# Kernel tuning notes

Hardware: AMD Instinct MI355X
Metric: run time of the kernel (lower is better)

The kernel has to match this reference:

```python
import jax, jax.numpy as jnp
import numpy as np

B, NPG, K, HID, MAXZ = 512, 256, 60, 128, 1000
NTOT = B * NPG            # 131072 nodes
DEG = 16
E = NTOT * DEG            # 2097152 edges
TLD = HID * 3 + 1         # 385 = total_latent_dim
DENSE = (K // 2 - 5 + 1) * 32  # 832


def setup_inputs() -> dict:
    key = jax.random.key(0)
    ks = jax.random.split(key, 20)
    # within-graph random edges, offset per graph
    loc = jax.random.randint(ks[0], (2, B, NPG * DEG), 0, NPG)
    offs = (jnp.arange(B) * NPG)[None, :, None]
    edge_index = (loc + offs).reshape(2, E).astype(jnp.int32)
    z = jax.random.randint(ks[1], (NTOT,), 0, MAXZ).astype(jnp.int32)
    edge_weight = jax.random.uniform(ks[2], (E,), dtype=jnp.float32)
    z_table = jax.random.normal(ks[3], (MAXZ, HID), dtype=jnp.float32) * 0.1
    W0 = jax.random.normal(ks[4], (HID, HID)) * 0.05
    W1 = jax.random.normal(ks[5], (HID, HID)) * 0.05
    W2 = jax.random.normal(ks[6], (HID, HID)) * 0.05
    W3 = jax.random.normal(ks[7], (HID, 1)) * 0.05
    b0 = jnp.zeros((HID,)); b1 = jnp.zeros((HID,)); b2 = jnp.zeros((HID,)); b3 = jnp.zeros((1,))
    conv1_w = jax.random.normal(ks[8], (16, 1, TLD)) * 0.05
    conv1_b = jnp.zeros((16,))
    conv2_w = jax.random.normal(ks[9], (32, 16, 5)) * 0.05
    conv2_b = jnp.zeros((32,))
    lin1_w = jax.random.normal(ks[10], (DENSE, 128)) * 0.05
    lin1_b = jnp.zeros((128,))
    lin2_w = jax.random.normal(ks[11], (128, 1)) * 0.05
    lin2_b = jnp.zeros((1,))
    return {"z_table": z_table, "W0": W0, "b0": b0, "W1": W1, "b1": b1,
            "W2": W2, "b2": b2, "W3": W3, "b3": b3,
            "conv1_w": conv1_w, "conv1_b": conv1_b, "conv2_w": conv2_w, "conv2_b": conv2_b,
            "lin1_w": lin1_w, "lin1_b": lin1_b, "lin2_w": lin2_w, "lin2_b": lin2_b,
            "edge_weight": edge_weight, "z": z, "edge_index": edge_index}


def reference(z_table, W0, b0, W1, b1, W2, b2, W3, b3,
              conv1_w, conv1_b, conv2_w, conv2_b,
              lin1_w, lin1_b, lin2_w, lin2_b,
              edge_weight, z, edge_index):
    # --- GCN normalization with self loops (symmetric) ---
    loops = jnp.arange(NTOT, dtype=edge_index.dtype)
    src = jnp.concatenate([edge_index[0], loops])
    dst = jnp.concatenate([edge_index[1], loops])
    ew = jnp.concatenate([edge_weight, jnp.ones((NTOT,), edge_weight.dtype)])
    deg = jax.ops.segment_sum(ew, dst, num_segments=NTOT)
    dinv = jnp.where(deg > 0, jax.lax.rsqrt(jnp.maximum(deg, 1e-12)), 0.0)
    norm = dinv[src] * ew * dinv[dst]

    def gcn(x, W, b):
        h = x @ W
        agg = jax.ops.segment_sum(h[src] * norm[:, None], dst, num_segments=NTOT)
        return agg + b

    x = z_table[z]                              # [NTOT, HID]
    xs = []
    for (W, b) in ((W0, b0), (W1, b1), (W2, b2), (W3, b3)):
        x = jnp.tanh(gcn(x, W, b))
        xs.append(x)
    x = jnp.concatenate(xs, axis=-1)            # [NTOT, 385]

    # --- global sort pool (descending by last channel, top-k per graph) ---
    xg = x.reshape(B, NPG, TLD)
    idx = jnp.argsort(-xg[:, :, -1], axis=1)[:, :K]
    pooled = jnp.take_along_axis(xg, idx[:, :, None], axis=1)   # [B, K, 385]
    y = pooled.reshape(B, 1, K * TLD)

    # --- dense conv1d / MLP head ---
    y = jax.lax.conv_general_dilated(y, conv1_w, (TLD,), 'VALID',
                                     dimension_numbers=('NCH', 'OIH', 'NCH'))
    y = jax.nn.relu(y + conv1_b[None, :, None])                  # [B,16,K]
    y = y.reshape(B, 16, K // 2, 2).max(axis=-1)                 # maxpool(2,2)
    y = jax.lax.conv_general_dilated(y, conv2_w, (1,), 'VALID',
                                     dimension_numbers=('NCH', 'OIH', 'NCH'))
    y = jax.nn.relu(y + conv2_b[None, :, None])                  # [B,32,26]
    y = y.reshape(B, -1)                                         # [B,832]
    y = jax.nn.relu(y @ lin1_w + lin1_b)
    return y @ lin2_w + lin2_b                                   # [B,1]
```

## Files before the change

kernel.cpp:

```cpp
#include <hip/hip_runtime.h>
#include <math.h>

#define NTOT   131072
#define NPG    256
#define BGR    512
#define HID    128
#define EDG    2097152
#define EPG    4096
#define EPGP   4864
#define KTOP   60
#define TLDIM  385

__device__ __forceinline__ int physX(int row, int c4) {
    return (c4 + row + (row >> 3)) & 31;
}
__device__ __forceinline__ int physA(int row, int c4) {
    return (c4 + (row >> 3) + ((row & 1) << 2)) & 31;
}

__global__ __launch_bounds__(1024, 4) void k_gnn(
        const float* __restrict__ zt, const int* __restrict__ z,
        const int* __restrict__ ei, const float* __restrict__ ew,
        const float* __restrict__ W0, const float* __restrict__ b0,
        const float* __restrict__ W1, const float* __restrict__ b1,
        const float* __restrict__ W2, const float* __restrict__ b2,
        const float* __restrict__ W3, const float* __restrict__ b3,
        float* __restrict__ X0, float* __restrict__ X1, float* __restrict__ X2,
        float* __restrict__ keyb, int* __restrict__ sel) {
    __shared__ float4 XS[NPG * 32];
    __shared__ __align__(16) float wnL[EPGP];
    __shared__ __align__(4) unsigned char esrcL[EPGP];
    __shared__ unsigned short offL[NPG + 1];
    __shared__ unsigned short mLn[NPG];
    __shared__ int    cntL[NPG];
    __shared__ float  selfnL[NPG];
    __shared__ float  dinvL[NPG];
    __shared__ float  t3s[NPG];
    __shared__ float  keyL[NPG];

    int t = threadIdx.x;
    int g = blockIdx.x;

    float*          ewL  = (float*)XS;
    unsigned char*  srcB = (unsigned char*)XS + 16384;
    unsigned char*  dstB = (unsigned char*)XS + 20480;
    unsigned short* hh   = (unsigned short*)((char*)XS + 24576);

    for (int j = t; j < EPG; j += 1024) {
        int e = g * EPG + j;
        ewL[j]  = ew[e];
        srcB[j] = (unsigned char)(ei[e] & (NPG - 1));
        dstB[j] = (unsigned char)(ei[EDG + e] & (NPG - 1));
    }
    for (int i = t; i < 64 * 256; i += 1024) hh[i] = 0;
    __syncthreads();
    if (t < 64) {
        int base = t * 64;
        unsigned short* hr = hh + t * 256;
        for (int i = 0; i < 64; i++) hr[dstB[base + i]]++;
    }
    __syncthreads();
    if (t < NPG) {
        int tot = 0;
        for (int c = 0; c < 64; c++) tot += hh[c * 256 + t];
        mLn[t]  = (unsigned short)tot;
        cntL[t] = (tot + 3) & ~3;
    }
    __syncthreads();
    if (t < 64) {
        int carry = 0;
        if (t == 0) offL[0] = 0;
        for (int seg = 0; seg < 4; seg++) {
            int v = cntL[seg * 64 + t];
#pragma unroll
            for (int d = 1; d < 64; d <<= 1) {
                int u = __shfl_up(v, d);
                if (t >= d) v += u;
            }
            offL[seg * 64 + t + 1] = (unsigned short)(v + carry);
            carry += __shfl(v, 63);
        }
    }
    __syncthreads();
    if (t < NPG) {
        int run = offL[t];
        for (int c = 0; c < 64; c++) {
            int tmp = hh[c * 256 + t];
            hh[c * 256 + t] = (unsigned short)run;
            run += tmp;
        }
    }
    __syncthreads();
    if (t < 64) {
        int base = t * 64;
        unsigned short* hr = hh + t * 256;
        for (int i = 0; i < 64; i++) {
            int e = base + i;
            int d = dstB[e];
            int slot = hr[d];
            hr[d] = (unsigned short)(slot + 1);
            esrcL[slot] = srcB[e];
            wnL[slot]   = ewL[e];
        }
    }
    __syncthreads();
    if (t < NPG) {
        int o = offL[t], m = mLn[t];
        float s = 0.f;
        for (int i = 0; i < m; i++) s += wnL[o + i];
        float dv = 1.0f / sqrtf(s + 1.0f);
        dinvL[t]  = dv;
        selfnL[t] = dv * dv;
    }
    __syncthreads();
    if (t < NPG) {
        int o = offL[t], m = mLn[t], pc = cntL[t];
        float dn = dinvL[t];
        for (int i = 0; i < m; i++)
            wnL[o + i] = dinvL[esrcL[o + i]] * wnL[o + i] * dn;
        for (int i = m; i < pc; i++) {
            esrcL[o + i] = (unsigned char)t;
            wnL[o + i]   = 0.f;
        }
    }
    __syncthreads();
    for (int i = t; i < NPG * 32; i += 1024) {
        int row = i >> 5, c4 = i & 31;
        int zi = z[g * NPG + row];
        XS[row * 32 + physX(row, c4)] = ((const float4*)zt)[(size_t)zi * 32 + c4];
    }
    __syncthreads();

    const unsigned int* esrcW = (const unsigned int*)esrcL;
    const float4*       wn4   = (const float4*)wnL;
    int wid  = t >> 6;
    int l    = t & 63;
    int half = l >> 5;
    int c4   = l & 31;
    int rg   = t & 31;
    int cgq  = t >> 5;

#pragma unroll 1
    for (int layer = 0; layer < 3; layer++) {
        const float* W    = (layer == 0) ? W0 : (layer == 1) ? W1 : W2;
        const float* bias = (layer == 0) ? b0 : (layer == 1) ? b1 : b2;
        float* Xout       = (layer == 0) ? X0 : (layer == 1) ? X1 : X2;

        float4 accA[8];
#pragma unroll 1
        for (int it = 0; it < 8; it++) {
            int p    = wid * 8 + it;
            int node = 2 * p + half;
            int oA = offL[2 * p], oM = offL[2 * p + 1], oE = offL[2 * p + 2];
            int m4A = (oM - oA) >> 2, m4B = (oE - oM) >> 2;
            int mmax4 = m4A > m4B ? m4A : m4B;
            int o4 = (half ? oM : oA) >> 2;
            int m4 = half ? m4B : m4A;
            unsigned int selfpack = (unsigned int)node * 0x01010101u;
            float4 acc = make_float4(0.f, 0.f, 0.f, 0.f);

            unsigned int s_cur = selfpack, s_nxt = selfpack;
            float4 w_cur = make_float4(0.f, 0.f, 0.f, 0.f);
            float4 w_nxt = make_float4(0.f, 0.f, 0.f, 0.f);
            float4 v0, v1, v2, v3;
            if (mmax4 > 0) {
                {
                    int jc = (0 < m4) ? 0 : 0;
                    int idx = o4 + jc;
                    unsigned int ss = esrcW[idx]; float4 ww = wn4[idx];
                    if (0 >= m4) { ss = selfpack; ww = make_float4(0.f,0.f,0.f,0.f); }
                    s_cur = ss; w_cur = ww;
                }
                {
                    int jc = (1 < m4) ? 1 : (m4 > 0 ? m4 - 1 : 0);
                    int idx = o4 + jc;
                    unsigned int ss = esrcW[idx]; float4 ww = wn4[idx];
                    if (1 >= m4) { ss = selfpack; ww = make_float4(0.f,0.f,0.f,0.f); }
                    s_nxt = ss; w_nxt = ww;
                }
                int a0 =  s_cur        & 255, a1 = (s_cur >> 8)  & 255;
                int a2i = (s_cur >> 16) & 255, a3 = (s_cur >> 24) & 255;
                v0 = XS[a0 * 32 + physX(a0, c4)];
                v1 = XS[a1 * 32 + physX(a1, c4)];
                v2 = XS[a2i * 32 + physX(a2i, c4)];
                v3 = XS[a3 * 32 + physX(a3, c4)];
            }
            for (int j4 = 0; j4 < mmax4; j4++) {
                int b0i =  s_nxt        & 255, b1i = (s_nxt >> 8)  & 255;
                int b2i = (s_nxt >> 16) & 255, b3i = (s_nxt >> 24) & 255;
                float4 n0 = XS[b0i * 32 + physX(b0i, c4)];
                float4 n1 = XS[b1i * 32 + physX(b1i, c4)];
                float4 n2 = XS[b2i * 32 + physX(b2i, c4)];
                float4 n3 = XS[b3i * 32 + physX(b3i, c4)];
                int jn = j4 + 2;
                int jc = (jn < m4) ? jn : (m4 > 0 ? m4 - 1 : 0);
                int idx = o4 + jc;
                unsigned int s2_ = esrcW[idx];
                float4 w2_ = wn4[idx];
                if (jn >= m4) { s2_ = selfpack; w2_ = make_float4(0.f,0.f,0.f,0.f); }
                acc.x += w_cur.x * v0.x; acc.y += w_cur.x * v0.y;
                acc.z += w_cur.x * v0.z; acc.w += w_cur.x * v0.w;
                acc.x += w_cur.y * v1.x; acc.y += w_cur.y * v1.y;
                acc.z += w_cur.y * v1.z; acc.w += w_cur.y * v1.w;
                acc.x += w_cur.z * v2.x; acc.y += w_cur.z * v2.y;
                acc.z += w_cur.z * v2.z; acc.w += w_cur.z * v2.w;
                acc.x += w_cur.w * v3.x; acc.y += w_cur.w * v3.y;
                acc.z += w_cur.w * v3.z; acc.w += w_cur.w * v3.w;
                v0 = n0; v1 = n1; v2 = n2; v3 = n3;
                w_cur = w_nxt; s_nxt = s2_; w_nxt = w2_;
            }
            float wsf = selfnL[node];
            float4 sv = XS[node * 32 + physX(node, c4)];
            acc.x += wsf * sv.x; acc.y += wsf * sv.y;
            acc.z += wsf * sv.z; acc.w += wsf * sv.w;
            accA[it] = acc;
        }
        __syncthreads();
#pragma unroll
        for (int it = 0; it < 8; it++) {
            int node = 2 * (wid * 8 + it) + half;
            XS[node * 32 + physA(node, c4)] = accA[it];
        }
        __syncthreads();

        float a2[8][4];
#pragma unroll
        for (int i = 0; i < 8; i++)
#pragma unroll
            for (int j = 0; j < 4; j++) a2[i][j] = 0.f;
        for (int k4 = 0; k4 < 32; k4++) {
            float4 a4[8];
#pragma unroll
            for (int i = 0; i < 8; i++) {
                int rl = rg * 8 + i;
                a4[i] = XS[rl * 32 + physA(rl, k4)];
            }
            float4 wv[4];
#pragma unroll
            for (int kw = 0; kw < 4; kw++)
                wv[kw] = *(((const float4*)(W + (size_t)(k4 * 4 + kw) * HID)) + cgq);
#pragma unroll
            for (int kw = 0; kw < 4; kw++) {
#pragma unroll
                for (int i = 0; i < 8; i++) {
                    float a = (kw == 0) ? a4[i].x : (kw == 1) ? a4[i].y
                            : (kw == 2) ? a4[i].z : a4[i].w;
                    a2[i][0] += a * wv[kw].x; a2[i][1] += a * wv[kw].y;
                    a2[i][2] += a * wv[kw].z; a2[i][3] += a * wv[kw].w;
                }
            }
        }
        float4 bv = ((const float4*)bias)[cgq];
        float4 oo[8];
#pragma unroll
        for (int i = 0; i < 8; i++) {
            oo[i].x = tanhf(a2[i][0] + bv.x); oo[i].y = tanhf(a2[i][1] + bv.y);
            oo[i].z = tanhf(a2[i][2] + bv.z); oo[i].w = tanhf(a2[i][3] + bv.w);
        }
        __syncthreads();
#pragma unroll
        for (int i = 0; i < 8; i++) {
            int rl = rg * 8 + i;
            XS[rl * 32 + physX(rl, cgq)] = oo[i];
        }
        __syncthreads();
        for (int i = t; i < NPG * 32; i += 1024) {
            int row = i >> 5, cc = i & 31;
            ((float4*)Xout)[(size_t)g * NPG * 32 + i] = XS[row * 32 + physX(row, cc)];
        }
    }

    {
        int n = t >> 2, part = t & 3;
        const float4* w4 = (const float4*)W3;
        const float4* rb = XS + n * 32;
        float s = 0.f;
#pragma unroll
        for (int q = 0; q < 8; q++) {
            float4 v = rb[physX(n, part * 8 + q)];
            float4 ww = w4[part * 8 + q];
            s += v.x * ww.x + v.y * ww.y + v.z * ww.z + v.w * ww.w;
        }
        s += __shfl_down(s, 2, 4);
        s += __shfl_down(s, 1, 4);
        if (part == 0) t3s[n] = s;
    }
    __syncthreads();

    if (t < NPG) {
        int o = offL[t], m2 = mLn[t];
        float s = 0.f;
        for (int i = 0; i < m2; i++)
            s += wnL[o + i] * t3s[esrcL[o + i]];
        s += selfnL[t] * t3s[t];
        float key = tanhf(s + b3[0]);
        keyL[t] = key;
        keyb[g * NPG + t] = key;
    }
    __syncthreads();
    if (t < NPG) {
        float ki = keyL[t];
        int rank = 0;
        for (int j = 0; j < NPG; j++) {
            float kj = keyL[j];
            rank += (kj > ki) || (kj == ki && j < t);
        }
        if (rank < KTOP) sel[g * KTOP + rank] = g * NPG + t;
    }
}

__global__ __launch_bounds__(256) void k_head(const float* __restrict__ X0,
                                              const float* __restrict__ X1,
                                              const float* __restrict__ X2,
                                              const float* __restrict__ key,
                                              const int* __restrict__ sel,
                                              const float* __restrict__ c1w,
                                              const float* __restrict__ c1b,
                                              const float* __restrict__ c2w,
                                              const float* __restrict__ c2b,
                                              const float* __restrict__ l1w,
                                              const float* __restrict__ l1b,
                                              const float* __restrict__ l2w,
                                              const float* __restrict__ l2b,
                                              float* __restrict__ out) {
    __shared__ __align__(16) float pch[KTOP * 132];
    __shared__ __align__(16) float w1s[16 * 132];
    __shared__ int   seln[KTOP];
    __shared__ float selk[KTOP];
    __shared__ float c1s[16 * KTOP];
    __shared__ float mps[16 * 30];
    __shared__ float w2s[32 * 80];
    __shared__ float yb[832];
    __shared__ float l1p[256];
    __shared__ float l1v[128];

    int g = blockIdx.x, t = threadIdx.x;
    if (t < KTOP) {
        int nd = sel[g * KTOP + t];
        seln[t] = nd;
        selk[t] = key[nd];
    }

    float acc1[4] = {0.f, 0.f, 0.f, 0.f};
    for (int tc = 0; tc < 3; tc++) {
        const float* Xsrc = (tc == 0) ? X0 : ((tc == 1) ? X1 : X2);
        __syncthreads();
        for (int i = t; i < KTOP * 32; i += 256) {
            int k = i >> 5, q = i & 31;
            int nd = seln[k];
            *((float4*)&pch[k * 132 + q * 4]) = ((const float4*)Xsrc)[(size_t)nd * 32 + q];
        }
        for (int i = t; i < 16 * 128; i += 256) {
            int ch = i >> 7, tt = i & 127;
            w1s[ch * 132 + tt] = c1w[ch * TLDIM + tc * 128 + tt];
        }
        __syncthreads();
#pragma unroll
        for (int it = 0; it < 4; it++) {
            int e = it * 256 + t;
            if (e < 960) {
                int k = e >> 4, ch = e & 15;
                const float* pr = &pch[k * 132];
                const float* wr = &w1s[ch * 132];
                float s = 0.f;
#pragma unroll
                for (int q = 0; q < 32; q++) {
                    float4 pv = *((float4*)&pr[q * 4]);
                    float4 wv = *((float4*)&wr[q * 4]);
                    s += pv.x * wv.x + pv.y * wv.y + pv.z * wv.z + pv.w * wv.w;
                }
                acc1[it] += s;
            }
        }
    }
    __syncthreads();
#pragma unroll
    for (int it = 0; it < 4; it++) {
        int e = it * 256 + t;
        if (e < 960) {
            int k = e >> 4, ch = e & 15;
            float v = acc1[it] + selk[k] * c1w[ch * TLDIM + 384] + c1b[ch];
            c1s[ch * KTOP + k] = fmaxf(v, 0.f);
        }
    }
    for (int i = t; i < 2560; i += 256) w2s[i] = c2w[i];
    __syncthreads();
    for (int i = t; i < 480; i += 256) {
        int ch = i / 30, p = i - ch * 30;
        mps[ch * 30 + p] = fmaxf(c1s[ch * KTOP + 2 * p], c1s[ch * KTOP + 2 * p + 1]);
    }
    __syncthreads();
    for (int e = t; e < 832; e += 256) {
        int oc = e / 26, q = e - oc * 26;
        float s = 0.f;
#pragma unroll
        for (int ic = 0; ic < 16; ic++) {
            const float* mr = &mps[ic * 30 + q];
            const float* wr = &w2s[oc * 80 + ic * 5];
#pragma unroll
            for (int j = 0; j < 5; j++) s += mr[j] * wr[j];
        }
        yb[e] = fmaxf(s + c2b[oc], 0.f);
    }
    __syncthreads();
    {
        int u = t & 127, h = t >> 7;
        float s = 0.f;
        for (int d = h * 416; d < h * 416 + 416; d++) s += yb[d] * l1w[d * 128 + u];
        l1p[t] = s;
    }
    __syncthreads();
    if (t < 128) {
        float v = fmaxf(l1p[t] + l1p[t + 128] + l1b[t], 0.f);
        l1v[t] = v * l2w[t];
    }
    __syncthreads();
    if (t < 64) {
        float v = l1v[t] + l1v[t + 64];
        v += __shfl_down(v, 32);
        v += __shfl_down(v, 16);
        v += __shfl_down(v, 8);
        v += __shfl_down(v, 4);
        v += __shfl_down(v, 2);
        v += __shfl_down(v, 1);
        if (t == 0) out[g] = v + l2b[0];
    }
}

extern "C" void kernel_launch(void* const* d_in, const int* in_sizes, int n_in,
                              void* d_out, int out_size, void* d_ws, size_t ws_size,
                              hipStream_t stream) {
    (void)in_sizes; (void)n_in; (void)out_size; (void)ws_size;
    const float* zt  = (const float*)d_in[0];
    const float* W0  = (const float*)d_in[1];
    const float* b0  = (const float*)d_in[2];
    const float* W1  = (const float*)d_in[3];
    const float* b1  = (const float*)d_in[4];
    const float* W2  = (const float*)d_in[5];
    const float* b2  = (const float*)d_in[6];
    const float* W3  = (const float*)d_in[7];
    const float* b3  = (const float*)d_in[8];
    const float* c1w = (const float*)d_in[9];
    const float* c1b = (const float*)d_in[10];
    const float* c2w = (const float*)d_in[11];
    const float* c2b = (const float*)d_in[12];
    const float* l1w = (const float*)d_in[13];
    const float* l1b = (const float*)d_in[14];
    const float* l2w = (const float*)d_in[15];
    const float* l2b = (const float*)d_in[16];
    const float* ew  = (const float*)d_in[17];
    const int*   z   = (const int*)d_in[18];
    const int*   ei  = (const int*)d_in[19];
    float* out = (float*)d_out;

    char* wsp = (char*)d_ws;
    size_t off = 0;
    auto alloc = [&](size_t bytes) -> void* {
        void* p = wsp + off;
        off += (bytes + 255) & ~(size_t)255;
        return p;
    };
    float* X0   = (float*)alloc((size_t)NTOT * HID * 4);
    float* X1   = (float*)alloc((size_t)NTOT * HID * 4);
    float* X2   = (float*)alloc((size_t)NTOT * HID * 4);
    float* keyb = (float*)alloc((size_t)NTOT * 4);
    int*   sel  = (int*)  alloc((size_t)BGR * KTOP * 4);

    k_gnn <<<BGR, dim3(1024), 0, stream>>>(zt, z, ei, ew,
                                           W0, b0, W1, b1, W2, b2, W3, b3,
                                           X0, X1, X2, keyb, sel);
    k_head<<<BGR, dim3(256), 0, stream>>>(X0, X1, X2, keyb, sel,
                                          c1w, c1b, c2w, c2b,
                                          l1w, l1b, l2w, l2b, out);
}
```

Measured before the change: 599.1 us.

## Fuse head into GNN kernel and keep layer-2 features in LDS

Merges the sort-pool/conv/MLP head into the GNN kernel so each block handles its own graph end to end. The third layer's output is read straight from shared memory instead of being written to global, and the key and selection buffers no longer go through global memory. The per-layer GEMM is remapped to a 4x8 register tile per thread, the histogram uses padded 32-bit counters to cut bank conflicts, and the remaining global stores are nontemporal. The trade-off is that the head now runs with 1024-thread blocks, with most threads idle in its later stages, and the shared-memory regions are reused under tight aliasing.

```diff
diff --git a/kernel.cpp b/kernel.cpp
--- a/kernel.cpp
+++ b/kernel.cpp
@@ -11,6 +11,8 @@
 #define KTOP   60
 #define TLDIM  385
 
+typedef float v4f __attribute__((ext_vector_type(4)));
+
 __device__ __forceinline__ int physX(int row, int c4) {
     return (c4 + row + (row >> 3)) & 31;
 }
@@ -25,18 +27,25 @@
         const float* __restrict__ W1, const float* __restrict__ b1,
         const float* __restrict__ W2, const float* __restrict__ b2,
         const float* __restrict__ W3, const float* __restrict__ b3,
-        float* __restrict__ X0, float* __restrict__ X1, float* __restrict__ X2,
-        float* __restrict__ keyb, int* __restrict__ sel) {
+        const float* __restrict__ c1w, const float* __restrict__ c1b,
+        const float* __restrict__ c2w, const float* __restrict__ c2b,
+        const float* __restrict__ l1w, const float* __restrict__ l1b,
+        const float* __restrict__ l2w, const float* __restrict__ l2b,
+        float* __restrict__ X0, float* __restrict__ X1,
+        float* __restrict__ out) {
     __shared__ float4 XS[NPG * 32];
-    __shared__ __align__(16) float wnL[EPGP];
-    __shared__ __align__(4) unsigned char esrcL[EPGP];
-    __shared__ unsigned short offL[NPG + 1];
+    __shared__ __align__(16) char HPOOL[24320];
+    __shared__ unsigned short offL[NPG + 2];
     __shared__ unsigned short mLn[NPG];
     __shared__ int    cntL[NPG];
     __shared__ float  selfnL[NPG];
     __shared__ float  dinvL[NPG];
     __shared__ float  t3s[NPG];
     __shared__ float  keyL[NPG];
+    __shared__ int    selN[KTOP];
+
+    float*         wnL   = (float*)HPOOL;
+    unsigned char* esrcL = (unsigned char*)(HPOOL + 19456);
 
     int t = threadIdx.x;
     int g = blockIdx.x;
@@ -44,7 +53,7 @@
     float*          ewL  = (float*)XS;
     unsigned char*  srcB = (unsigned char*)XS + 16384;
     unsigned char*  dstB = (unsigned char*)XS + 20480;
-    unsigned short* hh   = (unsigned short*)((char*)XS + 24576);
+    unsigned int*   hh   = (unsigned int*)((char*)XS + 24576);
 
     for (int j = t; j < EPG; j += 1024) {
         int e = g * EPG + j;
@@ -52,17 +61,17 @@
         srcB[j] = (unsigned char)(ei[e] & (NPG - 1));
         dstB[j] = (unsigned char)(ei[EDG + e] & (NPG - 1));
     }
-    for (int i = t; i < 64 * 256; i += 1024) hh[i] = 0;
+    for (int i = t; i < 64 * 257; i += 1024) hh[i] = 0;
     __syncthreads();
     if (t < 64) {
         int base = t * 64;
-        unsigned short* hr = hh + t * 256;
+        unsigned int* hr = hh + t * 257;
         for (int i = 0; i < 64; i++) hr[dstB[base + i]]++;
     }
     __syncthreads();
     if (t < NPG) {
         int tot = 0;
-        for (int c = 0; c < 64; c++) tot += hh[c * 256 + t];
+        for (int c = 0; c < 64; c++) tot += hh[c * 257 + t];
         mLn[t]  = (unsigned short)tot;
         cntL[t] = (tot + 3) & ~3;
     }
@@ -85,20 +94,20 @@
     if (t < NPG) {
         int run = offL[t];
         for (int c = 0; c < 64; c++) {
-            int tmp = hh[c * 256 + t];
-            hh[c * 256 + t] = (unsigned short)run;
+            int tmp = hh[c * 257 + t];
+            hh[c * 257 + t] = (unsigned int)run;
             run += tmp;
         }
     }
     __syncthreads();
     if (t < 64) {
         int base = t * 64;
-        unsigned short* hr = hh + t * 256;
+        unsigned int* hr = hh + t * 257;
         for (int i = 0; i < 64; i++) {
             int e = base + i;
             int d = dstB[e];
             int slot = hr[d];
-            hr[d] = (unsigned short)(slot + 1);
+            hr[d] = slot + 1;
             esrcL[slot] = srcB[e];
             wnL[slot]   = ewL[e];
         }
@@ -137,14 +146,15 @@
     int l    = t & 63;
     int half = l >> 5;
     int c4   = l & 31;
-    int rg   = t & 31;
-    int cgq  = t >> 5;
+    int rowg = t & 63;
+    int colg = t >> 6;
+    int cq0 = colg * 2, cq1 = cq0 + 1;
 
 #pragma unroll 1
     for (int layer = 0; layer < 3; layer++) {
         const float* W    = (layer == 0) ? W0 : (layer == 1) ? W1 : W2;
         const float* bias = (layer == 0) ? b0 : (layer == 1) ? b1 : b2;
-        float* Xout       = (layer == 0) ? X0 : (layer == 1) ? X1 : X2;
+        float* Xout       = (layer == 0) ? X0 : (layer == 1) ? X1 : nullptr;
 
         float4 accA[8];
 #pragma unroll 1
@@ -165,8 +175,7 @@
             float4 v0, v1, v2, v3;
             if (mmax4 > 0) {
                 {
-                    int jc = (0 < m4) ? 0 : 0;
-                    int idx = o4 + jc;
+                    int idx = o4;
                     unsigned int ss = esrcW[idx]; float4 ww = wn4[idx];
                     if (0 >= m4) { ss = selfpack; ww = make_float4(0.f,0.f,0.f,0.f); }
                     s_cur = ss; w_cur = ww;
@@ -223,50 +232,60 @@
         }
         __syncthreads();
 
-        float a2[8][4];
-#pragma unroll
-        for (int i = 0; i < 8; i++)
-#pragma unroll
-            for (int j = 0; j < 4; j++) a2[i][j] = 0.f;
+        float a2[4][8];
+#pragma unroll
+        for (int i = 0; i < 4; i++)
+#pragma unroll
+            for (int j = 0; j < 8; j++) a2[i][j] = 0.f;
         for (int k4 = 0; k4 < 32; k4++) {
-            float4 a4[8];
-#pragma unroll
-            for (int i = 0; i < 8; i++) {
-                int rl = rg * 8 + i;
+            float4 a4[4];
+#pragma unroll
+            for (int i = 0; i < 4; i++) {
+                int rl = rowg * 4 + i;
                 a4[i] = XS[rl * 32 + physA(rl, k4)];
             }
-            float4 wv[4];
-#pragma unroll
-            for (int kw = 0; kw < 4; kw++)
-                wv[kw] = *(((const float4*)(W + (size_t)(k4 * 4 + kw) * HID)) + cgq);
 #pragma unroll
             for (int kw = 0; kw < 4; kw++) {
-#pragma unroll
-                for (int i = 0; i < 8; i++) {
+                const float4* wp = (const float4*)(W + (size_t)(k4 * 4 + kw) * HID);
+                float4 wv0 = wp[cq0];
+                float4 wv1 = wp[cq1];
+#pragma unroll
+                for (int i = 0; i < 4; i++) {
                     float a = (kw == 0) ? a4[i].x : (kw == 1) ? a4[i].y
                             : (kw == 2) ? a4[i].z : a4[i].w;
-                    a2[i][0] += a * wv[kw].x; a2[i][1] += a * wv[kw].y;
-                    a2[i][2] += a * wv[kw].z; a2[i][3] += a * wv[kw].w;
+                    a2[i][0] += a * wv0.x; a2[i][1] += a * wv0.y;
+                    a2[i][2] += a * wv0.z; a2[i][3] += a * wv0.w;
+                    a2[i][4] += a * wv1.x; a2[i][5] += a * wv1.y;
+                    a2[i][6] += a * wv1.z; a2[i][7] += a * wv1.w;
                 }
             }
         }
-        float4 bv = ((const float4*)bias)[cgq];
-        float4 oo[8];
-#pragma unroll
-        for (int i = 0; i < 8; i++) {
-            oo[i].x = tanhf(a2[i][0] + bv.x); oo[i].y = tanhf(a2[i][1] + bv.y);
-            oo[i].z = tanhf(a2[i][2] + bv.z); oo[i].w = tanhf(a2[i][3] + bv.w);
+        float4 bv0 = ((const float4*)bias)[cq0];
+        float4 bv1 = ((const float4*)bias)[cq1];
+        float4 o0[4], o1[4];
+#pragma unroll
+        for (int i = 0; i < 4; i++) {
+            o0[i].x = tanhf(a2[i][0] + bv0.x); o0[i].y = tanhf(a2[i][1] + bv0.y);
+            o0[i].z = tanhf(a2[i][2] + bv0.z); o0[i].w = tanhf(a2[i][3] + bv0.w);
+            o1[i].x = tanhf(a2[i][4] + bv1.x); o1[i].y = tanhf(a2[i][5] + bv1.y);
+            o1[i].z = tanhf(a2[i][6] + bv1.z); o1[i].w = tanhf(a2[i][7] + bv1.w);
         }
         __syncthreads();
 #pragma unroll
-        for (int i = 0; i < 8; i++) {
-            int rl = rg * 8 + i;
-            XS[rl * 32 + physX(rl, cgq)] = oo[i];
+        for (int i = 0; i < 4; i++) {
+            int rl = rowg * 4 + i;
+            XS[rl * 32 + physX(rl, cq0)] = o0[i];
+            XS[rl * 32 + physX(rl, cq1)] = o1[i];
         }
         __syncthreads();
-        for (int i = t; i < NPG * 32; i += 1024) {
-            int row = i >> 5, cc = i & 31;
-            ((float4*)Xout)[(size_t)g * NPG * 32 + i] = XS[row * 32 + physX(row, cc)];
+        if (Xout) {
+            v4f* dst = (v4f*)Xout + (size_t)g * NPG * 32;
+            for (int i = t; i < NPG * 32; i += 1024) {
+                int row = i >> 5, cc = i & 31;
+                float4 val = XS[row * 32 + physX(row, cc)];
+                v4f vv; vv.x = val.x; vv.y = val.y; vv.z = val.z; vv.w = val.w;
+                __builtin_nontemporal_store(vv, dst + i);
+            }
         }
     }
 
@@ -293,9 +312,7 @@
         for (int i = 0; i < m2; i++)
             s += wnL[o + i] * t3s[esrcL[o + i]];
         s += selfnL[t] * t3s[t];
-        float key = tanhf(s + b3[0]);
-        keyL[t] = key;
-        keyb[g * NPG + t] = key;
+        keyL[t] = tanhf(s + b3[0]);
     }
     __syncthreads();
     if (t < NPG) {
@@ -305,93 +322,71 @@
             float kj = keyL[j];
             rank += (kj > ki) || (kj == ki && j < t);
         }
-        if (rank < KTOP) sel[g * KTOP + rank] = g * NPG + t;
-    }
-}
-
-__global__ __launch_bounds__(256) void k_head(const float* __restrict__ X0,
-                                              const float* __restrict__ X1,
-                                              const float* __restrict__ X2,
-                                              const float* __restrict__ key,
-                                              const int* __restrict__ sel,
-                                              const float* __restrict__ c1w,
-                                              const float* __restrict__ c1b,
-                                              const float* __restrict__ c2w,
-                                              const float* __restrict__ c2b,
-                                              const float* __restrict__ l1w,
-                                              const float* __restrict__ l1b,
-                                              const float* __restrict__ l2w,
-                                              const float* __restrict__ l2b,
-                                              float* __restrict__ out) {
-    __shared__ __align__(16) float pch[KTOP * 132];
-    __shared__ __align__(16) float w1s[16 * 132];
-    __shared__ int   seln[KTOP];
-    __shared__ float selk[KTOP];
-    __shared__ float c1s[16 * KTOP];
-    __shared__ float mps[16 * 30];
-    __shared__ float w2s[32 * 80];
-    __shared__ float yb[832];
-    __shared__ float l1p[256];
-    __shared__ float l1v[128];
-
-    int g = blockIdx.x, t = threadIdx.x;
-    if (t < KTOP) {
-        int nd = sel[g * KTOP + t];
-        seln[t] = nd;
-        selk[t] = key[nd];
-    }
-
-    float acc1[4] = {0.f, 0.f, 0.f, 0.f};
+        if (rank < KTOP) selN[rank] = t;
+    }
+    __threadfence();
+    __syncthreads();
+
+    float4* pch4 = (float4*)HPOOL;
+    float4* w1s4 = (float4*)(HPOOL + 15872);
+    float*  c1s  = (float*)HPOOL;
+    float*  mps  = (float*)(HPOOL + 3840);
+    float*  w2s  = (float*)(HPOOL + 5760);
+    float*  yb   = (float*)(HPOOL + 16000);
+    float*  l1p  = (float*)(HPOOL + 19328);
+    float*  l1v  = (float*)(HPOOL + 20352);
+
+    float acc1 = 0.f;
+    int hk = t >> 4, hch = t & 15;
+#pragma unroll 1
     for (int tc = 0; tc < 3; tc++) {
-        const float* Xsrc = (tc == 0) ? X0 : ((tc == 1) ? X1 : X2);
+        const float* Xsrc = (tc == 0) ? X0 : X1;
         __syncthreads();
-        for (int i = t; i < KTOP * 32; i += 256) {
-            int k = i >> 5, q = i & 31;
-            int nd = seln[k];
-            *((float4*)&pch[k * 132 + q * 4]) = ((const float4*)Xsrc)[(size_t)nd * 32 + q];
-        }
-        for (int i = t; i < 16 * 128; i += 256) {
+        for (int i = t; i < 16 * 128; i += 1024) {
             int ch = i >> 7, tt = i & 127;
-            w1s[ch * 132 + tt] = c1w[ch * TLDIM + tc * 128 + tt];
-        }
-        __syncthreads();
-#pragma unroll
-        for (int it = 0; it < 4; it++) {
-            int e = it * 256 + t;
-            if (e < 960) {
-                int k = e >> 4, ch = e & 15;
-                const float* pr = &pch[k * 132];
-                const float* wr = &w1s[ch * 132];
+            ((float*)w1s4)[ch * 132 + tt] = c1w[ch * TLDIM + tc * 128 + tt];
+        }
+#pragma unroll 1
+        for (int kk = 0; kk < 2; kk++) {
+            __syncthreads();
+            if (t < 960) {
+                int k2 = t >> 5, q = t & 31;
+                int nd = selN[kk * 30 + k2];
+                float4 v;
+                if (tc < 2) v = ((const float4*)Xsrc)[((size_t)(g * NPG + nd)) * 32 + q];
+                else        v = XS[nd * 32 + physX(nd, q)];
+                pch4[k2 * 33 + q] = v;
+            }
+            __syncthreads();
+            if (t < 960 && hk >= kk * 30 && hk < kk * 30 + 30) {
+                int lr = hk - kk * 30;
+                const float4* pr = pch4 + lr * 33;
+                const float4* wr = w1s4 + hch * 33;
                 float s = 0.f;
 #pragma unroll
                 for (int q = 0; q < 32; q++) {
-                    float4 pv = *((float4*)&pr[q * 4]);
-                    float4 wv = *((float4*)&wr[q * 4]);
+                    float4 pv = pr[q];
+                    float4 wv = wr[q];
                     s += pv.x * wv.x + pv.y * wv.y + pv.z * wv.z + pv.w * wv.w;
                 }
-                acc1[it] += s;
-            }
-        }
-    }
-    __syncthreads();
-#pragma unroll
-    for (int it = 0; it < 4; it++) {
-        int e = it * 256 + t;
-        if (e < 960) {
-            int k = e >> 4, ch = e & 15;
-            float v = acc1[it] + selk[k] * c1w[ch * TLDIM + 384] + c1b[ch];
-            c1s[ch * KTOP + k] = fmaxf(v, 0.f);
-        }
-    }
-    for (int i = t; i < 2560; i += 256) w2s[i] = c2w[i];
-    __syncthreads();
-    for (int i = t; i < 480; i += 256) {
-        int ch = i / 30, p = i - ch * 30;
+                acc1 += s;
+            }
+        }
+    }
+    __syncthreads();
+    if (t < 960) {
+        float v = acc1 + keyL[selN[hk]] * c1w[hch * TLDIM + 384] + c1b[hch];
+        c1s[hch * KTOP + hk] = fmaxf(v, 0.f);
+    }
+    for (int i = t; i < 2560; i += 1024) w2s[i] = c2w[i];
+    __syncthreads();
+    if (t < 480) {
+        int ch = t / 30, p = t - ch * 30;
         mps[ch * 30 + p] = fmaxf(c1s[ch * KTOP + 2 * p], c1s[ch * KTOP + 2 * p + 1]);
     }
     __syncthreads();
-    for (int e = t; e < 832; e += 256) {
-        int oc = e / 26, q = e - oc * 26;
+    if (t < 832) {
+        int oc = t / 26, q = t - oc * 26;
         float s = 0.f;
 #pragma unroll
         for (int ic = 0; ic < 16; ic++) {
@@ -400,10 +395,10 @@
 #pragma unroll
             for (int j = 0; j < 5; j++) s += mr[j] * wr[j];
         }
-        yb[e] = fmaxf(s + c2b[oc], 0.f);
-    }
-    __syncthreads();
-    {
+        yb[t] = fmaxf(s + c2b[oc], 0.f);
+    }
+    __syncthreads();
+    if (t < 256) {
         int u = t & 127, h = t >> 7;
         float s = 0.f;
         for (int d = h * 416; d < h * 416 + 416; d++) s += yb[d] * l1w[d * 128 + u];
@@ -460,16 +455,12 @@
         off += (bytes + 255) & ~(size_t)255;
         return p;
     };
-    float* X0   = (float*)alloc((size_t)NTOT * HID * 4);
-    float* X1   = (float*)alloc((size_t)NTOT * HID * 4);
-    float* X2   = (float*)alloc((size_t)NTOT * HID * 4);
-    float* keyb = (float*)alloc((size_t)NTOT * 4);
-    int*   sel  = (int*)  alloc((size_t)BGR * KTOP * 4);
-
-    k_gnn <<<BGR, dim3(1024), 0, stream>>>(zt, z, ei, ew,
-                                           W0, b0, W1, b1, W2, b2, W3, b3,
-                                           X0, X1, X2, keyb, sel);
-    k_head<<<BGR, dim3(256), 0, stream>>>(X0, X1, X2, keyb, sel,
+    float* X0 = (float*)alloc((size_t)NTOT * HID * 4);
+    float* X1 = (float*)alloc((size_t)NTOT * HID * 4);
+
+    k_gnn<<<BGR, dim3(1024), 0, stream>>>(zt, z, ei, ew,
+                                          W0, b0, W1, b1, W2, b2, W3, b3,
                                           c1w, c1b, c2w, c2b,
-                                          l1w, l1b, l2w, l2b, out);
+                                          l1w, l1b, l2w, l2b,
+                                          X0, X1, out);
 }
```

Result: slower. 687.3 us (+14.7%).

## Write only top-k rows of last GCN layer and pack selection output

Applied to the files above, without the earlier changes.

Instead of writing the full third-layer node features to global memory, the GNN kernel now writes only the 60 selected rows per graph into a compact buffer, along with the selected keys and local indices. The head kernel reads that packed buffer directly, which removes a full-size feature write and the indirect key lookup. The per-chunk histogram also moves from 16-bit to 32-bit counters with a padded stride of 257, aimed at reducing LDS bank conflicts. The trade-off is a little more shared memory and an extra barrier in the GNN kernel.

```diff
diff --git a/kernel.cpp b/kernel.cpp
--- a/kernel.cpp
+++ b/kernel.cpp
@@ -25,18 +25,19 @@
         const float* __restrict__ W1, const float* __restrict__ b1,
         const float* __restrict__ W2, const float* __restrict__ b2,
         const float* __restrict__ W3, const float* __restrict__ b3,
-        float* __restrict__ X0, float* __restrict__ X1, float* __restrict__ X2,
-        float* __restrict__ keyb, int* __restrict__ sel) {
+        float* __restrict__ X0, float* __restrict__ X1,
+        float* __restrict__ P2, float* __restrict__ selK, int* __restrict__ selI) {
     __shared__ float4 XS[NPG * 32];
     __shared__ __align__(16) float wnL[EPGP];
     __shared__ __align__(4) unsigned char esrcL[EPGP];
-    __shared__ unsigned short offL[NPG + 1];
+    __shared__ unsigned short offL[NPG + 2];
     __shared__ unsigned short mLn[NPG];
     __shared__ int    cntL[NPG];
     __shared__ float  selfnL[NPG];
     __shared__ float  dinvL[NPG];
     __shared__ float  t3s[NPG];
     __shared__ float  keyL[NPG];
+    __shared__ int    selN[KTOP];
 
     int t = threadIdx.x;
     int g = blockIdx.x;
@@ -44,7 +45,7 @@
     float*          ewL  = (float*)XS;
     unsigned char*  srcB = (unsigned char*)XS + 16384;
     unsigned char*  dstB = (unsigned char*)XS + 20480;
-    unsigned short* hh   = (unsigned short*)((char*)XS + 24576);
+    unsigned int*   hh   = (unsigned int*)((char*)XS + 24576);
 
     for (int j = t; j < EPG; j += 1024) {
         int e = g * EPG + j;
@@ -52,17 +53,17 @@
         srcB[j] = (unsigned char)(ei[e] & (NPG - 1));
         dstB[j] = (unsigned char)(ei[EDG + e] & (NPG - 1));
     }
-    for (int i = t; i < 64 * 256; i += 1024) hh[i] = 0;
+    for (int i = t; i < 64 * 257; i += 1024) hh[i] = 0;
     __syncthreads();
     if (t < 64) {
         int base = t * 64;
-        unsigned short* hr = hh + t * 256;
+        unsigned int* hr = hh + t * 257;
         for (int i = 0; i < 64; i++) hr[dstB[base + i]]++;
     }
     __syncthreads();
     if (t < NPG) {
         int tot = 0;
-        for (int c = 0; c < 64; c++) tot += hh[c * 256 + t];
+        for (int c = 0; c < 64; c++) tot += hh[c * 257 + t];
         mLn[t]  = (unsigned short)tot;
         cntL[t] = (tot + 3) & ~3;
     }
@@ -85,20 +86,20 @@
     if (t < NPG) {
         int run = offL[t];
         for (int c = 0; c < 64; c++) {
-            int tmp = hh[c * 256 + t];
-            hh[c * 256 + t] = (unsigned short)run;
+            int tmp = hh[c * 257 + t];
+            hh[c * 257 + t] = (unsigned int)run;
             run += tmp;
         }
     }
     __syncthreads();
     if (t < 64) {
         int base = t * 64;
-        unsigned short* hr = hh + t * 256;
+        unsigned int* hr = hh + t * 257;
         for (int i = 0; i < 64; i++) {
             int e = base + i;
             int d = dstB[e];
             int slot = hr[d];
-            hr[d] = (unsigned short)(slot + 1);
+            hr[d] = slot + 1;
             esrcL[slot] = srcB[e];
             wnL[slot]   = ewL[e];
         }
@@ -137,14 +138,14 @@
     int l    = t & 63;
     int half = l >> 5;
     int c4   = l & 31;
-    int rg   = t & 31;
-    int cgq  = t >> 5;
+    int rg  = t & 31;
+    int cgq = t >> 5;
 
 #pragma unroll 1
     for (int layer = 0; layer < 3; layer++) {
         const float* W    = (layer == 0) ? W0 : (layer == 1) ? W1 : W2;
         const float* bias = (layer == 0) ? b0 : (layer == 1) ? b1 : b2;
-        float* Xout       = (layer == 0) ? X0 : (layer == 1) ? X1 : X2;
+        float* Xout       = (layer == 0) ? X0 : (layer == 1) ? X1 : nullptr;
 
         float4 accA[8];
 #pragma unroll 1
@@ -165,8 +166,7 @@
             float4 v0, v1, v2, v3;
             if (mmax4 > 0) {
                 {
-                    int jc = (0 < m4) ? 0 : 0;
-                    int idx = o4 + jc;
+                    int idx = o4;
                     unsigned int ss = esrcW[idx]; float4 ww = wn4[idx];
                     if (0 >= m4) { ss = selfpack; ww = make_float4(0.f,0.f,0.f,0.f); }
                     s_cur = ss; w_cur = ww;
@@ -264,9 +264,12 @@
             XS[rl * 32 + physX(rl, cgq)] = oo[i];
         }
         __syncthreads();
-        for (int i = t; i < NPG * 32; i += 1024) {
-            int row = i >> 5, cc = i & 31;
-            ((float4*)Xout)[(size_t)g * NPG * 32 + i] = XS[row * 32 + physX(row, cc)];
+        if (Xout) {
+            float4* dst = (float4*)Xout + (size_t)g * NPG * 32;
+            for (int i = t; i < NPG * 32; i += 1024) {
+                int row = i >> 5, cc = i & 31;
+                dst[i] = XS[row * 32 + physX(row, cc)];
+            }
         }
     }
 
@@ -293,9 +296,7 @@
         for (int i = 0; i < m2; i++)
             s += wnL[o + i] * t3s[esrcL[o + i]];
         s += selfnL[t] * t3s[t];
-        float key = tanhf(s + b3[0]);
-        keyL[t] = key;
-        keyb[g * NPG + t] = key;
+        keyL[t] = tanhf(s + b3[0]);
     }
     __syncthreads();
     if (t < NPG) {
@@ -305,15 +306,26 @@
             float kj = keyL[j];
             rank += (kj > ki) || (kj == ki && j < t);
         }
-        if (rank < KTOP) sel[g * KTOP + rank] = g * NPG + t;
+        if (rank < KTOP) selN[rank] = t;
+    }
+    __syncthreads();
+    if (t < KTOP) {
+        int nd = selN[t];
+        selI[g * KTOP + t] = nd;
+        selK[g * KTOP + t] = keyL[nd];
+    }
+    for (int i = t; i < KTOP * 32; i += 1024) {
+        int r = i >> 5, q = i & 31;
+        int nd = selN[r];
+        ((float4*)P2)[(size_t)g * KTOP * 32 + i] = XS[nd * 32 + physX(nd, q)];
     }
 }
 
 __global__ __launch_bounds__(256) void k_head(const float* __restrict__ X0,
                                               const float* __restrict__ X1,
-                                              const float* __restrict__ X2,
-                                              const float* __restrict__ key,
-                                              const int* __restrict__ sel,
+                                              const float* __restrict__ P2,
+                                              const float* __restrict__ selK,
+                                              const int* __restrict__ selI,
                                               const float* __restrict__ c1w,
                                               const float* __restrict__ c1b,
                                               const float* __restrict__ c2w,
@@ -336,19 +348,24 @@
 
     int g = blockIdx.x, t = threadIdx.x;
     if (t < KTOP) {
-        int nd = sel[g * KTOP + t];
-        seln[t] = nd;
-        selk[t] = key[nd];
+        seln[t] = selI[g * KTOP + t];
+        selk[t] = selK[g * KTOP + t];
     }
 
     float acc1[4] = {0.f, 0.f, 0.f, 0.f};
     for (int tc = 0; tc < 3; tc++) {
-        const float* Xsrc = (tc == 0) ? X0 : ((tc == 1) ? X1 : X2);
+        const float* Xsrc = (tc == 0) ? X0 : X1;
         __syncthreads();
         for (int i = t; i < KTOP * 32; i += 256) {
             int k = i >> 5, q = i & 31;
-            int nd = seln[k];
-            *((float4*)&pch[k * 132 + q * 4]) = ((const float4*)Xsrc)[(size_t)nd * 32 + q];
+            float4 v;
+            if (tc < 2) {
+                int nd = seln[k];
+                v = ((const float4*)Xsrc)[((size_t)g * NPG + nd) * 32 + q];
+            } else {
+                v = ((const float4*)P2)[(size_t)g * KTOP * 32 + i];
+            }
+            *((float4*)&pch[k * 132 + q * 4]) = v;
         }
         for (int i = t; i < 16 * 128; i += 256) {
             int ch = i >> 7, tt = i & 127;
@@ -462,14 +479,14 @@
     };
     float* X0   = (float*)alloc((size_t)NTOT * HID * 4);
     float* X1   = (float*)alloc((size_t)NTOT * HID * 4);
-    float* X2   = (float*)alloc((size_t)NTOT * HID * 4);
-    float* keyb = (float*)alloc((size_t)NTOT * 4);
-    int*   sel  = (int*)  alloc((size_t)BGR * KTOP * 4);
+    float* P2   = (float*)alloc((size_t)BGR * KTOP * HID * 4);
+    float* selK = (float*)alloc((size_t)BGR * KTOP * 4);
+    int*   selI = (int*)  alloc((size_t)BGR * KTOP * 4);
 
     k_gnn <<<BGR, dim3(1024), 0, stream>>>(zt, z, ei, ew,
                                            W0, b0, W1, b1, W2, b2, W3, b3,
-                                           X0, X1, X2, keyb, sel);
-    k_head<<<BGR, dim3(256), 0, stream>>>(X0, X1, X2, keyb, sel,
+                                           X0, X1, P2, selK, selI);
+    k_head<<<BGR, dim3(256), 0, stream>>>(X0, X1, P2, selK, selI,
                                           c1w, c1b, c2w, c2b,
                                           l1w, l1b, l2w, l2b, out);
 }
```

Result: faster. 585.7 us (-2.2%).
